# Optimization experiments

Hardware: AMD Instinct MI355X
Metric: run time of the kernel (lower is better)

Reference implementation:

```python
import jax, jax.numpy as jnp
import numpy as np

THRESHOLD = 0.3
EPS = 1e-8  # matches torch F.cosine_similarity eps


def _normalize(x):
    # L2-normalize rows with torch-style eps clamp on the norm
    n = jnp.sqrt(jnp.sum(x * x, axis=-1, keepdims=True))
    return x / jnp.maximum(n, EPS)


def _triu_cos_self(x):
    # pairwise cosine similarity of x with itself, upper triangle (offset=1)
    xn = _normalize(x)
    csm = xn @ xn.T  # [N, N]
    i, j = jnp.triu_indices(x.shape[0], k=1)
    return csm[i, j]


def setup_inputs() -> dict:
    key = jax.random.key(0)
    k1, k2 = jax.random.split(key)
    stereos = jax.random.normal(k1, (96, 768), dtype=jnp.float32)
    astereos = jax.random.normal(k2, (96, 768), dtype=jnp.float32)
    return {"stereos": stereos, "astereos": astereos}


def reference(stereos, astereos):
    # positive sims: triu of each self cosine-similarity matrix, concatenated
    pos_sim = jnp.concatenate(
        [_triu_cos_self(stereos), _triu_cos_self(astereos)], axis=0
    )  # [P]
    # negative sims: full cross cosine similarity, flattened
    neg = _normalize(astereos) @ _normalize(stereos).T  # [M, N]
    neg_sim = neg.reshape(-1)  # [Q]
    # hinge over the full pos x neg outer product: mean(max(0, neg - pos + thr))
    diff = neg_sim[None, :] - pos_sim[:, None] + THRESHOLD  # [P, Q]
    return jnp.mean(jnp.maximum(diff, 0.0))
```

## Files before the change

kernel.cpp:

```cpp
#include <hip/hip_runtime.h>
#include <math.h>

#define NROWS   96
#define DIM     768
#define THRESH  0.3f
#define NPAIR   4560
#define PTOT    9120
#define QTOT    9216
#define NBLK    576
#define NWAVES  (NBLK * 4)
#define SPR     24

#define AST(p, v) __hip_atomic_store((p), (v), __ATOMIC_RELAXED, __HIP_MEMORY_SCOPE_AGENT)
#define ALD(p)    __hip_atomic_load((p), __ATOMIC_RELAXED, __HIP_MEMORY_SCOPE_AGENT)


__device__ __forceinline__ float d12(
    const float4& x0, const float4& x1, const float4& x2,
    const float4& y0, const float4& y1, const float4& y2)
{
    return x0.x*y0.x + x0.y*y0.y + x0.z*y0.z + x0.w*y0.w
         + x1.x*y1.x + x1.y*y1.y + x1.z*y1.z + x1.w*y1.w
         + x2.x*y2.x + x2.y*y2.y + x2.z*y2.z + x2.w*y2.w;
}

template <int N>
__device__ __forceinline__ void wreduce(float* v)
{
#pragma unroll
    for (int off = 32; off; off >>= 1) {
#pragma unroll
        for (int k = 0; k < N; k++) v[k] += __shfl_down(v[k], off);
    }
}

__global__ __launch_bounds__(256) void fused_kernel(
    const float* __restrict__ stereos, const float* __restrict__ astereos,
    float* __restrict__ pos, float* __restrict__ neg,
    float* __restrict__ slotSp, float* __restrict__ slotSn,
    float* __restrict__ slotMx, float* __restrict__ slotMn,
    unsigned int* __restrict__ ctr, const unsigned int* __restrict__ ref,
    float* __restrict__ out)
{
    __shared__ float  sSp[4], sSn[4], sMx[4], sMn[4];
    __shared__ int    sLast;
    __shared__ double rsp[4], rsn[4], redd[4];
    __shared__ float  rmx[4], rmn[4];
    __shared__ double bcd[2];
    __shared__ float  bnmin;
    __shared__ int    rare;
    __shared__ float  sNeg[QTOT];

    int tid  = threadIdx.x;
    int wave = tid >> 6, lane = tid & 63;
    int gw = blockIdx.x * 4 + wave;
    int i  = gw / SPR;
    int j0 = (gw - i * SPR) * 4;

    float acc[13];
    {
        const float4* aS = (const float4*)(stereos  + i * DIM);
        const float4* aC = (const float4*)(astereos + i * DIM);
        float4 as0 = aS[lane], as1 = aS[lane + 64], as2 = aS[lane + 128];
        float4 ac0 = aC[lane], ac1 = aC[lane + 64], ac2 = aC[lane + 128];
        acc[0] = d12(as0, as1, as2, as0, as1, as2);
        acc[1] = d12(ac0, ac1, ac2, ac0, ac1, ac2);
#pragma unroll
        for (int m = 0; m < 4; m++) {
            const float4* b = (const float4*)(stereos + (j0 + m) * DIM);
            float4 b0 = b[lane], b1 = b[lane + 64], b2 = b[lane + 128];
            acc[2 + m]  = d12(b0, b1, b2, b0, b1, b2);
            acc[6 + m]  = d12(as0, as1, as2, b0, b1, b2);
            acc[10 + m] = d12(ac0, ac1, ac2, b0, b1, b2);
        }
        wreduce<13>(acc);
    }
    int sw = NWAVES - 1 - gw;
    int ia = sw / SPR, ja0 = (sw - ia * SPR) * 4;
    float accA[9];
    {
        const float4* aA = (const float4*)(astereos + ia * DIM);
        float4 a0 = aA[lane], a1 = aA[lane + 64], a2 = aA[lane + 128];
        accA[0] = d12(a0, a1, a2, a0, a1, a2);
#pragma unroll
        for (int m = 0; m < 4; m++) {
            const float4* b = (const float4*)(astereos + (ja0 + m) * DIM);
            float4 b0 = b[lane], b1 = b[lane + 64], b2 = b[lane + 128];
            accA[1 + m] = d12(b0, b1, b2, b0, b1, b2);
            accA[5 + m] = d12(a0, a1, a2, b0, b1, b2);
        }
        wreduce<9>(accA);
    }

    if (lane == 0) {
        float wsp = 0.f, wsn = 0.f, wmx = -INFINITY, wmn = INFINITY;
        float invaS = 1.0f / fmaxf(sqrtf(acc[0]), 1e-8f);
        float invaC = 1.0f / fmaxf(sqrtf(acc[1]), 1e-8f);
        int baseS = (i * (191 - i)) / 2 - i - 1;
#pragma unroll
        for (int m = 0; m < 4; m++) {
            float invb = 1.0f / fmaxf(sqrtf(acc[2 + m]), 1e-8f);
            float sc = acc[10 + m] * invaC * invb;
            AST(&neg[i * NROWS + j0 + m], sc);
            wsn += sc; wmn = fminf(wmn, sc);
            if (j0 + m > i) {
                float ss = acc[6 + m] * invaS * invb;
                AST(&pos[baseS + j0 + m], ss);
                wsp += ss; wmx = fmaxf(wmx, ss);
            }
        }
        float invaA = 1.0f / fmaxf(sqrtf(accA[0]), 1e-8f);
        int baseA = (ia * (191 - ia)) / 2 - ia - 1;
#pragma unroll
        for (int m = 0; m < 4; m++) {
            if (ja0 + m > ia) {
                float invb = 1.0f / fmaxf(sqrtf(accA[1 + m]), 1e-8f);
                float sa = accA[5 + m] * invaA * invb;
                AST(&pos[NPAIR + baseA + ja0 + m], sa);
                wsp += sa; wmx = fmaxf(wmx, sa);
            }
        }
        sSp[wave] = wsp; sSn[wave] = wsn; sMx[wave] = wmx; sMn[wave] = wmn;
    }
    __syncthreads();

    if (tid == 0) {
        AST(&slotSp[blockIdx.x], sSp[0] + sSp[1] + sSp[2] + sSp[3]);
        AST(&slotSn[blockIdx.x], sSn[0] + sSn[1] + sSn[2] + sSn[3]);
        AST(&slotMx[blockIdx.x], fmaxf(fmaxf(sMx[0], sMx[1]), fmaxf(sMx[2], sMx[3])));
        AST(&slotMn[blockIdx.x], fminf(fminf(sMn[0], sMn[1]), fminf(sMn[2], sMn[3])));
        asm volatile("s_waitcnt vmcnt(0)" ::: "memory");
        unsigned int base = *ref;
        unsigned int old  = atomicAdd(ctr, 1u);
        sLast = (((old - base) % (unsigned)NBLK) == (unsigned)(NBLK - 1));
    }
    __syncthreads();
    if (!sLast) return;

    double sp = 0.0, sn = 0.0;
    float mx = -INFINITY, mn = INFINITY;
    for (int f = tid; f < NBLK; f += 256) {
        sp += (double)ALD(&slotSp[f]);
        sn += (double)ALD(&slotSn[f]);
        mx = fmaxf(mx, ALD(&slotMx[f]));
        mn = fminf(mn, ALD(&slotMn[f]));
    }
    for (int off = 32; off; off >>= 1) {
        sp += __shfl_down(sp, off);
        sn += __shfl_down(sn, off);
        mx = fmaxf(mx, __shfl_down(mx, off));
        mn = fminf(mn, __shfl_down(mn, off));
    }
    if (lane == 0) { rsp[wave] = sp; rsn[wave] = sn;
                     rmx[wave] = mx; rmn[wave] = mn; }
    __syncthreads();
    if (tid == 0) {
        bcd[0] = rsp[0] + rsp[1] + rsp[2] + rsp[3];
        bcd[1] = rsn[0] + rsn[1] + rsn[2] + rsn[3];
        float pm = fmaxf(fmaxf(rmx[0], rmx[1]), fmaxf(rmx[2], rmx[3]));
        float nm = fminf(fminf(rmn[0], rmn[1]), fminf(rmn[2], rmn[3]));
        bnmin = nm;
        rare = (pm - nm > THRESH) ? 1 : 0;
    }
    __syncthreads();

    double corr = 0.0;
    if (rare) {
        for (int q = tid; q < QTOT; q += 256) sNeg[q] = ALD(&neg[q]);
        __syncthreads();
        float nmv = bnmin;
        for (int p = tid; p < PTOT; p += 256) {
            float pv = ALD(&pos[p]);
            if (pv - nmv > THRESH) {
                for (int q = 0; q < QTOT; q++) {
                    float d = pv - THRESH - sNeg[q];
                    if (d > 0.f) corr += (double)d;
                }
            }
        }
    }
    for (int off = 32; off; off >>= 1) corr += __shfl_down(corr, off);
    if (lane == 0) redd[wave] = corr;
    __syncthreads();
    if (tid == 0) {
        corr = redd[0] + redd[1] + redd[2] + redd[3];
        double PQ = (double)PTOT * (double)QTOT;
        double total = (double)PTOT * bcd[1] - (double)QTOT * bcd[0]
                     + PQ * (double)THRESH + corr;
        out[0] = (float)(total / PQ);
    }
}

extern "C" void kernel_launch(void* const* d_in, const int* in_sizes, int n_in,
                              void* d_out, int out_size, void* d_ws, size_t ws_size,
                              hipStream_t stream)
{
    const float* stereos  = (const float*)d_in[0];
    const float* astereos = (const float*)d_in[1];

    char* ws = (char*)d_ws;
    float* pos    = (float*)ws;
    float* neg    = (float*)(ws + 36480);
    float* slotSp = (float*)(ws + 73344);
    float* slotSn = (float*)(ws + 75648);
    float* slotMx = (float*)(ws + 77952);
    float* slotMn = (float*)(ws + 80256);

    size_t ctr_off = (ws_size >= (1u << 19) + 4) ? (size_t)(1u << 18) : 82944u;
    size_t ref_off = (ws_size >= (1u << 19) + 4) ? (size_t)(1u << 19) : 87040u;
    unsigned int* ctr = (unsigned int*)(ws + ctr_off);
    const unsigned int* ref = (const unsigned int*)(ws + ref_off);

    fused_kernel<<<NBLK, 256, 0, stream>>>(stereos, astereos, pos, neg,
                                           slotSp, slotSn, slotMx, slotMn,
                                           ctr, ref, (float*)d_out);
}
```

Measured before the change: 65.55 us.

## Replace per-wave dot products with 32x32 LDS-tiled Gram blocks over 21 tiles

Stacks both inputs into one 192-row matrix and computes its Gram matrix. Each of 21 blocks handles one upper-triangle 32x32 tile, staging K-chunks of rows in shared memory with padded strides. Row norms are computed from the same staged data. This replaces 576 blocks of wave-level dot products that re-read global rows and did many shuffle reductions. The rare-path correction loop stays as it was and now reuses the tile buffer for its negative-sim cache. The grid drops to 21 blocks, so far fewer compute units are used.

Result: slower. 76.83 us (+17.2%).

```diff
diff --git a/kernel.cpp b/kernel.cpp
--- a/kernel.cpp
+++ b/kernel.cpp
@@ -1,40 +1,39 @@
 #include <hip/hip_runtime.h>
 #include <math.h>
 
-#define NROWS   96
-#define DIM     768
-#define THRESH  0.3f
-#define NPAIR   4560
-#define PTOT    9120
-#define QTOT    9216
-#define NBLK    576
-#define NWAVES  (NBLK * 4)
-#define SPR     24
+#define NROWS    96
+#define DIM      768
+#define THRESH   0.3f
+#define NPAIR    4560
+#define PTOT     9120
+#define QTOT     9216
+#define NTILE    21
+#define TDIM     32
+#define KCH      384
+#define RSTRIDE  388
 
 #define AST(p, v) __hip_atomic_store((p), (v), __ATOMIC_RELAXED, __HIP_MEMORY_SCOPE_AGENT)
 #define ALD(p)    __hip_atomic_load((p), __ATOMIC_RELAXED, __HIP_MEMORY_SCOPE_AGENT)
 
 
-__device__ __forceinline__ float d12(
-    const float4& x0, const float4& x1, const float4& x2,
-    const float4& y0, const float4& y1, const float4& y2)
-{
-    return x0.x*y0.x + x0.y*y0.y + x0.z*y0.z + x0.w*y0.w
-         + x1.x*y1.x + x1.y*y1.y + x1.z*y1.z + x1.w*y1.w
-         + x2.x*y2.x + x2.y*y2.y + x2.z*y2.z + x2.w*y2.w;
-}
-
 template <int N>
-__device__ __forceinline__ void wreduce(float* v)
+__device__ __forceinline__ void wreduce2(float* s, float* mx, float* mn)
 {
 #pragma unroll
     for (int off = 32; off; off >>= 1) {
 #pragma unroll
-        for (int k = 0; k < N; k++) v[k] += __shfl_down(v[k], off);
-    }
-}
-
-__global__ __launch_bounds__(256) void fused_kernel(
+        for (int k = 0; k < N; k++) s[k] += __shfl_down(s[k], off);
+        *mx = fmaxf(*mx, __shfl_down(*mx, off));
+        *mn = fminf(*mn, __shfl_down(*mn, off));
+    }
+}
+
+__device__ __forceinline__ float dot4(const float4& a, const float4& b)
+{
+    return a.x*b.x + a.y*b.y + a.z*b.z + a.w*b.w;
+}
+
+__global__ __launch_bounds__(256) void gram_fused(
     const float* __restrict__ stereos, const float* __restrict__ astereos,
     float* __restrict__ pos, float* __restrict__ neg,
     float* __restrict__ slotSp, float* __restrict__ slotSn,
@@ -42,85 +41,128 @@
     unsigned int* __restrict__ ctr, const unsigned int* __restrict__ ref,
     float* __restrict__ out)
 {
-    __shared__ float  sSp[4], sSn[4], sMx[4], sMn[4];
-    __shared__ int    sLast;
+    __shared__ float bufR[TDIM * RSTRIDE];
+    __shared__ float bufC[TDIM * RSTRIDE];
+    __shared__ float pnrm[64][4];
+    __shared__ float invn[64];
+    __shared__ float sSp[4], sSn[4], sMx[4], sMn[4];
+    __shared__ int   sLast;
     __shared__ double rsp[4], rsn[4], redd[4];
     __shared__ float  rmx[4], rmn[4];
     __shared__ double bcd[2];
     __shared__ float  bnmin;
     __shared__ int    rare;
-    __shared__ float  sNeg[QTOT];
 
     int tid  = threadIdx.x;
     int wave = tid >> 6, lane = tid & 63;
-    int gw = blockIdx.x * 4 + wave;
-    int i  = gw / SPR;
-    int j0 = (gw - i * SPR) * 4;
-
-    float acc[13];
+
+    unsigned int base = 0;
+    if (tid == 0) base = ALD(ref);
+
+    int b = blockIdx.x, bi = 0;
+    while (b >= 6 - bi) { b -= 6 - bi; bi++; }
+    int bj  = bi + b;
+    int gri = bi * TDIM;
+    int grj = bj * TDIM;
+    const float* srcR = (gri < NROWS) ? (stereos  + gri * DIM)
+                                      : (astereos + (gri - NROWS) * DIM);
+    const float* srcC = (grj < NROWS) ? (stereos  + grj * DIM)
+                                      : (astereos + (grj - NROWS) * DIM);
+
+    int cc = lane & 31;
+    int r0 = wave * 8 + (lane >> 5) * 4;
+
+    float acc[4] = {0.f, 0.f, 0.f, 0.f};
+    float np = 0.f;
+    int nrow = tid & 63, npart = tid >> 6;
+
+    for (int kc = 0; kc < 2; kc++) {
+        {
+            int srow = tid >> 3;
+            int sc0  = tid & 7;
+            const float4* gR = (const float4*)(srcR + srow * DIM + kc * KCH);
+            const float4* gC = (const float4*)(srcC + srow * DIM + kc * KCH);
+            float4* lR = (float4*)(bufR + srow * RSTRIDE);
+            float4* lC = (float4*)(bufC + srow * RSTRIDE);
+#pragma unroll
+            for (int j = 0; j < 12; j++) {
+                lR[sc0 + 8 * j] = gR[sc0 + 8 * j];
+                lC[sc0 + 8 * j] = gC[sc0 + 8 * j];
+            }
+        }
+        __syncthreads();
+
+        {
+            const float4* rp = (const float4*)(nrow < TDIM
+                ? bufR + nrow * RSTRIDE : bufC + (nrow - TDIM) * RSTRIDE);
+#pragma unroll
+            for (int j = 0; j < 24; j++) {
+                float4 v = rp[npart * 24 + j];
+                np += v.x*v.x + v.y*v.y + v.z*v.z + v.w*v.w;
+            }
+        }
+
+        {
+            const float4* cp  = (const float4*)(bufC + cc * RSTRIDE);
+            const float4* rp0 = (const float4*)(bufR + (r0 + 0) * RSTRIDE);
+            const float4* rp1 = (const float4*)(bufR + (r0 + 1) * RSTRIDE);
+            const float4* rp2 = (const float4*)(bufR + (r0 + 2) * RSTRIDE);
+            const float4* rp3 = (const float4*)(bufR + (r0 + 3) * RSTRIDE);
+#pragma unroll 8
+            for (int k4 = 0; k4 < KCH / 4; k4++) {
+                float4 xc = cp[k4];
+                acc[0] += dot4(rp0[k4], xc);
+                acc[1] += dot4(rp1[k4], xc);
+                acc[2] += dot4(rp2[k4], xc);
+                acc[3] += dot4(rp3[k4], xc);
+            }
+        }
+        __syncthreads();
+    }
+
+    pnrm[nrow][npart] = np;
+    __syncthreads();
+    if (tid < 64) {
+        float s = pnrm[tid][0] + pnrm[tid][1] + pnrm[tid][2] + pnrm[tid][3];
+        invn[tid] = 1.0f / fmaxf(sqrtf(s), 1e-8f);
+    }
+    __syncthreads();
+
+    float wsp = 0.f, wsn = 0.f, wmx = -INFINITY, wmn = INFINITY;
     {
-        const float4* aS = (const float4*)(stereos  + i * DIM);
-        const float4* aC = (const float4*)(astereos + i * DIM);
-        float4 as0 = aS[lane], as1 = aS[lane + 64], as2 = aS[lane + 128];
-        float4 ac0 = aC[lane], ac1 = aC[lane + 64], ac2 = aC[lane + 128];
-        acc[0] = d12(as0, as1, as2, as0, as1, as2);
-        acc[1] = d12(ac0, ac1, ac2, ac0, ac1, ac2);
+        int colsInA = (grj >= NROWS);
+        int rowsInA = (gri >= NROWS);
+        float ivc = invn[TDIM + cc];
+        int gj = grj + cc;
 #pragma unroll
         for (int m = 0; m < 4; m++) {
-            const float4* b = (const float4*)(stereos + (j0 + m) * DIM);
-            float4 b0 = b[lane], b1 = b[lane + 64], b2 = b[lane + 128];
-            acc[2 + m]  = d12(b0, b1, b2, b0, b1, b2);
-            acc[6 + m]  = d12(as0, as1, as2, b0, b1, b2);
-            acc[10 + m] = d12(ac0, ac1, ac2, b0, b1, b2);
-        }
-        wreduce<13>(acc);
-    }
-    int sw = NWAVES - 1 - gw;
-    int ia = sw / SPR, ja0 = (sw - ia * SPR) * 4;
-    float accA[9];
+            int rl = r0 + m;
+            int gi = gri + rl;
+            float sim = acc[m] * invn[rl] * ivc;
+            if (colsInA) {
+                if (rowsInA) {
+                    if (gj > gi) {
+                        int ai = gi - NROWS, aj = gj - NROWS;
+                        AST(&pos[NPAIR + (ai * (191 - ai)) / 2 - ai - 1 + aj], sim);
+                        wsp += sim; wmx = fmaxf(wmx, sim);
+                    }
+                } else {
+                    AST(&neg[(gj - NROWS) * NROWS + gi], sim);
+                    wsn += sim; wmn = fminf(wmn, sim);
+                }
+            } else {
+                if (gj > gi) {
+                    AST(&pos[(gi * (191 - gi)) / 2 - gi - 1 + gj], sim);
+                    wsp += sim; wmx = fmaxf(wmx, sim);
+                }
+            }
+        }
+    }
     {
-        const float4* aA = (const float4*)(astereos + ia * DIM);
-        float4 a0 = aA[lane], a1 = aA[lane + 64], a2 = aA[lane + 128];
-        accA[0] = d12(a0, a1, a2, a0, a1, a2);
-#pragma unroll
-        for (int m = 0; m < 4; m++) {
-            const float4* b = (const float4*)(astereos + (ja0 + m) * DIM);
-            float4 b0 = b[lane], b1 = b[lane + 64], b2 = b[lane + 128];
-            accA[1 + m] = d12(b0, b1, b2, b0, b1, b2);
-            accA[5 + m] = d12(a0, a1, a2, b0, b1, b2);
-        }
-        wreduce<9>(accA);
-    }
-
-    if (lane == 0) {
-        float wsp = 0.f, wsn = 0.f, wmx = -INFINITY, wmn = INFINITY;
-        float invaS = 1.0f / fmaxf(sqrtf(acc[0]), 1e-8f);
-        float invaC = 1.0f / fmaxf(sqrtf(acc[1]), 1e-8f);
-        int baseS = (i * (191 - i)) / 2 - i - 1;
-#pragma unroll
-        for (int m = 0; m < 4; m++) {
-            float invb = 1.0f / fmaxf(sqrtf(acc[2 + m]), 1e-8f);
-            float sc = acc[10 + m] * invaC * invb;
-            AST(&neg[i * NROWS + j0 + m], sc);
-            wsn += sc; wmn = fminf(wmn, sc);
-            if (j0 + m > i) {
-                float ss = acc[6 + m] * invaS * invb;
-                AST(&pos[baseS + j0 + m], ss);
-                wsp += ss; wmx = fmaxf(wmx, ss);
-            }
-        }
-        float invaA = 1.0f / fmaxf(sqrtf(accA[0]), 1e-8f);
-        int baseA = (ia * (191 - ia)) / 2 - ia - 1;
-#pragma unroll
-        for (int m = 0; m < 4; m++) {
-            if (ja0 + m > ia) {
-                float invb = 1.0f / fmaxf(sqrtf(accA[1 + m]), 1e-8f);
-                float sa = accA[5 + m] * invaA * invb;
-                AST(&pos[NPAIR + baseA + ja0 + m], sa);
-                wsp += sa; wmx = fmaxf(wmx, sa);
-            }
-        }
-        sSp[wave] = wsp; sSn[wave] = wsn; sMx[wave] = wmx; sMn[wave] = wmn;
+        float s2[2] = {wsp, wsn};
+        wreduce2<2>(s2, &wmx, &wmn);
+        if (lane == 0) { sSp[wave] = s2[0]; sSn[wave] = s2[1];
+                         sMx[wave] = wmx;   sMn[wave] = wmn; }
     }
     __syncthreads();
 
@@ -130,16 +172,15 @@
         AST(&slotMx[blockIdx.x], fmaxf(fmaxf(sMx[0], sMx[1]), fmaxf(sMx[2], sMx[3])));
         AST(&slotMn[blockIdx.x], fminf(fminf(sMn[0], sMn[1]), fminf(sMn[2], sMn[3])));
         asm volatile("s_waitcnt vmcnt(0)" ::: "memory");
-        unsigned int base = *ref;
-        unsigned int old  = atomicAdd(ctr, 1u);
-        sLast = (((old - base) % (unsigned)NBLK) == (unsigned)(NBLK - 1));
+        unsigned int old = atomicAdd(ctr, 1u);
+        sLast = (((old - base) % (unsigned)NTILE) == (unsigned)(NTILE - 1));
     }
     __syncthreads();
     if (!sLast) return;
 
     double sp = 0.0, sn = 0.0;
     float mx = -INFINITY, mn = INFINITY;
-    for (int f = tid; f < NBLK; f += 256) {
+    for (int f = tid; f < NTILE; f += 256) {
         sp += (double)ALD(&slotSp[f]);
         sn += (double)ALD(&slotSn[f]);
         mx = fmaxf(mx, ALD(&slotMx[f]));
@@ -166,6 +207,7 @@
 
     double corr = 0.0;
     if (rare) {
+        float* sNeg = bufR;
         for (int q = tid; q < QTOT; q += 256) sNeg[q] = ALD(&neg[q]);
         __syncthreads();
         float nmv = bnmin;
@@ -206,12 +248,18 @@
     float* slotMx = (float*)(ws + 77952);
     float* slotMn = (float*)(ws + 80256);
 
-    size_t ctr_off = (ws_size >= (1u << 19) + 4) ? (size_t)(1u << 18) : 82944u;
-    size_t ref_off = (ws_size >= (1u << 19) + 4) ? (size_t)(1u << 19) : 87040u;
+    size_t ctr_off, ref_off;
+    if (ws_size >= (1u << 19) + 4) {
+        ctr_off = (size_t)1 << 18;
+        ref_off = (size_t)1 << 19;
+    } else {
+        ctr_off = 82688;
+        ref_off = 82944;
+    }
     unsigned int* ctr = (unsigned int*)(ws + ctr_off);
     const unsigned int* ref = (const unsigned int*)(ws + ref_off);
 
-    fused_kernel<<<NBLK, 256, 0, stream>>>(stereos, astereos, pos, neg,
-                                           slotSp, slotSn, slotMx, slotMn,
-                                           ctr, ref, (float*)d_out);
-}
+    gram_fused<<<NTILE, 256, 0, stream>>>(stereos, astereos, pos, neg,
+                                          slotSp, slotSn, slotMx, slotMn,
+                                          ctr, ref, (float*)d_out);
+}
```
